# Kernel tuning notes

Hardware: AMD Instinct MI355X
Metric: run time of the kernel (lower is better)

Reference implementation:

```python
import jax, jax.numpy as jnp
import numpy as np

N_NODES = 500_000
N_EDGES = 8_000_000
N_GRAPHS = 512
N_FEATURES = 128
HIDDEN = 128
N_FILT = 8
OUT_DIM = 64
BN_EPS = 1e-5


def setup_inputs() -> dict:
    key = jax.random.key(0)
    ks = jax.random.split(key, 16)
    rn = lambda k, shape, s=0.05: jax.random.normal(k, shape, jnp.float32) * s
    return {
        "x": jax.random.normal(ks[0], (N_NODES, N_FEATURES), jnp.float32),
        "W1": rn(ks[1], (N_FEATURES, HIDDEN)),
        "b1": jnp.zeros((HIDDEN,), jnp.float32),
        "W2": rn(ks[2], (HIDDEN, N_FILT)),
        "b2": jnp.zeros((N_FILT,), jnp.float32),
        "W0": rn(ks[3], (2 * N_FILT, OUT_DIM)),
        "b0": jnp.zeros((OUT_DIM,), jnp.float32),
        "g1W": rn(ks[4], (OUT_DIM, OUT_DIM)),
        "g1b": jnp.zeros((OUT_DIM,), jnp.float32),
        "l1W": rn(ks[5], (OUT_DIM, OUT_DIM)),
        "g2W": rn(ks[6], (OUT_DIM, N_FEATURES)),
        "g2b": jnp.zeros((N_FEATURES,), jnp.float32),
        "l2W": rn(ks[7], (OUT_DIM, N_FEATURES)),
        "bn_gamma": jnp.ones((N_FEATURES,), jnp.float32),
        "bn_beta": jnp.zeros((N_FEATURES,), jnp.float32),
        "edge_index": jax.random.randint(ks[8], (2, N_EDGES), 0, N_NODES),
        "batch": jnp.sort(jax.random.randint(ks[9], (N_NODES,), 0, N_GRAPHS)),
        "death_edge_idx": jax.random.randint(ks[10], (N_NODES,), 0, N_EDGES),
    }


def _deepset(x, batch, GW, Gb, LW):
    # scatter-mean over graphs, Linear (no bias), gather-broadcast subtract
    sums = jax.ops.segment_sum(x, batch, num_segments=N_GRAPHS)  # [G, d]
    cnt = jax.ops.segment_sum(jnp.ones((x.shape[0], 1), x.dtype), batch,
                              num_segments=N_GRAPHS)             # [G, 1]
    xm = (sums / jnp.maximum(cnt, 1.0)) @ LW                      # Lambda
    return x @ GW + Gb - xm[batch]                                # Gamma - gather


def reference(x, W1, b1, W2, b2, W0, b0, g1W, g1b, l1W, g2W, g2b, l2W,
              bn_gamma, bn_beta, edge_index, batch, death_edge_idx):
    # filtrations MLP: [N, F] -> [N, n_filtrations]
    filtered_v = jax.nn.relu(x @ W1 + b1) @ W2 + b2
    # edge filtration = max of endpoint values (gather + max), [E, n_filtrations]
    filtered_e = jnp.maximum(filtered_v[edge_index[0]], filtered_v[edge_index[1]])
    # persistence pairs (lower-star 0-dim generators): birth = vertex value,
    # death = paired edge value; layout [N, n_filt, 2] -> [N, 2*n_filt]
    births = filtered_v
    deaths = filtered_e[death_edge_idx]
    x0 = jnp.stack([births, deaths], axis=-1).reshape(x.shape[0], 2 * N_FILT)
    # set_fn: Linear -> ReLU -> DeepSet -> ReLU -> DeepSet
    x0 = jax.nn.relu(x0 @ W0 + b0)
    x0 = jax.nn.relu(_deepset(x0, batch, g1W, g1b, l1W))
    x0 = _deepset(x0, batch, g2W, g2b, l2W)
    # residual: x + BatchNorm1d(relu(x0)) with batch statistics
    h = jax.nn.relu(x0)
    mu = h.mean(axis=0)
    var = h.var(axis=0)
    hn = (h - mu) * jax.lax.rsqrt(var + BN_EPS)
    return x + hn * bn_gamma + bn_beta
```

## Files before the change

kernel.cpp:

```cpp
#include <hip/hip_runtime.h>
#include <hip/hip_bf16.h>

#define NNODES 500000
#define NEDGES 8000000
#define NGRAPHS 512
#define NFEAT 128
#define NHID 128
#define NFILT 8
#define ODIM 64
#define BN_EPS 1e-5f
#define NBLK2 3907
#define NBLK3 7813

typedef __attribute__((ext_vector_type(8))) short bf16x8;
typedef __attribute__((ext_vector_type(4))) float f32x4;
#define MFMA16(a, b, c) __builtin_amdgcn_mfma_f32_16x16x32_bf16(a, b, c, 0, 0, 0)

__device__ inline ushort f2bs(float f) {
  union { __hip_bfloat16 h; ushort u; } cv;
  cv.h = __float2bfloat16(f);
  return cv.u;
}

__global__ void k_pack(const float* __restrict__ g1W, const float* __restrict__ g2W,
                       const float* __restrict__ W1,
                       ushort* __restrict__ pW1, ushort* __restrict__ pW2,
                       ushort* __restrict__ pW0) {
  int idx = blockIdx.x * 256 + threadIdx.x;
  if (idx < 4096) {
    int j = idx & 7, l = (idx >> 3) & 63, kb = (idx >> 9) & 1, ncb = idx >> 10;
    int k = kb * 32 + (l >> 4) * 8 + j, c = ncb * 16 + (l & 15);
    pW1[idx] = f2bs(g1W[k * 64 + c]);
  }
  if (idx < 8192) {
    int j = idx & 7, l = (idx >> 3) & 63, kb = (idx >> 9) & 1, ncb = idx >> 10;
    int k = kb * 32 + (l >> 4) * 8 + j, c = ncb * 16 + (l & 15);
    pW2[idx] = f2bs(g2W[k * 128 + c]);
  }
  if (idx < 16384) {
    int j = idx & 7, l = (idx >> 3) & 63, kb = (idx >> 9) & 3, ncb = idx >> 11;
    int k = kb * 32 + (l >> 4) * 8 + j, c = ncb * 16 + (l & 15);
    pW0[idx] = f2bs(W1[k * 128 + c]);
  }
}

__global__ __launch_bounds__(256) void k_filt(
    const float* __restrict__ x, const ushort* __restrict__ pW0,
    const float* __restrict__ b1, const float* __restrict__ W2,
    const float* __restrict__ b2, float* __restrict__ fv) {
  __shared__ float w2s[128 * 12];
  const int t = threadIdx.x;
  for (int i = t; i < 1024; i += 256) {
    int c = i >> 3, f = i & 7;
    w2s[c * 12 + f] = W2[i];
  }
  __syncthreads();
  const int wv = t >> 6, l = t & 63;
  const int lr = l & 15, lg = l >> 4;
  const int n0 = blockIdx.x * 128 + wv * 32;
  if (n0 >= NNODES) return;

  union { uint4 u; bf16x8 b; } bf[2][4];
#pragma unroll
  for (int mt = 0; mt < 2; ++mt)
#pragma unroll
    for (int kb = 0; kb < 4; ++kb) {
      const float* src = &x[(size_t)(n0 + mt * 16 + lr) * 128 + kb * 32 + lg * 8];
      float v[8];
      *(float4*)&v[0] = *(const float4*)src;
      *(float4*)&v[4] = *(const float4*)(src + 4);
      ushort s[8];
#pragma unroll
      for (int e = 0; e < 8; ++e) s[e] = f2bs(v[e]);
      bf[mt][kb].u = *(uint4*)s;
    }

  float pf0[8], pf1[8];
#pragma unroll
  for (int f = 0; f < 8; ++f) { pf0[f] = 0.f; pf1[f] = 0.f; }

#pragma unroll
  for (int ncb = 0; ncb < 8; ++ncb) {
    union { uint4 u; bf16x8 b; } af[4];
#pragma unroll
    for (int kb = 0; kb < 4; ++kb)
      af[kb].u = *(const uint4*)&pW0[((ncb * 4 + kb) * 64 + l) * 8];
    f32x4 a0 = (f32x4){0.f, 0.f, 0.f, 0.f};
    f32x4 a1 = (f32x4){0.f, 0.f, 0.f, 0.f};
#pragma unroll
    for (int kb = 0; kb < 4; ++kb) {
      a0 = MFMA16(af[kb].b, bf[0][kb].b, a0);
      a1 = MFMA16(af[kb].b, bf[1][kb].b, a1);
    }
    float bbv[4];
    *(float4*)bbv = *(const float4*)&b1[ncb * 16 + lg * 4];
#pragma unroll
    for (int r = 0; r < 4; ++r) {
      const int c = ncb * 16 + lg * 4 + r;
      float h0 = fmaxf(a0[r] + bbv[r], 0.f);
      float h1 = fmaxf(a1[r] + bbv[r], 0.f);
      float w20[4], w21[4];
      *(float4*)w20 = *(const float4*)&w2s[c * 12];
      *(float4*)w21 = *(const float4*)&w2s[c * 12 + 4];
#pragma unroll
      for (int f = 0; f < 4; ++f) {
        pf0[f]     = fmaf(h0, w20[f], pf0[f]);
        pf0[f + 4] = fmaf(h0, w21[f], pf0[f + 4]);
        pf1[f]     = fmaf(h1, w20[f], pf1[f]);
        pf1[f + 4] = fmaf(h1, w21[f], pf1[f + 4]);
      }
    }
  }
#pragma unroll
  for (int f = 0; f < 8; ++f) {
    pf0[f] += __shfl_xor(pf0[f], 16); pf0[f] += __shfl_xor(pf0[f], 32);
    pf1[f] += __shfl_xor(pf1[f], 16); pf1[f] += __shfl_xor(pf1[f], 32);
  }
  if (lg == 0) {
    float o0[8], o1[8];
#pragma unroll
    for (int f = 0; f < 8; ++f) {
      float bb = b2[f];
      o0[f] = pf0[f] + bb;
      o1[f] = pf1[f] + bb;
    }
    *(float4*)&fv[(size_t)(n0 + lr) * 8]          = *(float4*)&o0[0];
    *(float4*)&fv[(size_t)(n0 + lr) * 8 + 4]      = *(float4*)&o0[4];
    *(float4*)&fv[(size_t)(n0 + 16 + lr) * 8]     = *(float4*)&o1[0];
    *(float4*)&fv[(size_t)(n0 + 16 + lr) * 8 + 4] = *(float4*)&o1[4];
  }
}

__global__ void k_bounds(const int* __restrict__ batch, int* __restrict__ cnt) {
  int g = blockIdx.x * 64 + threadIdx.x;
  if (g >= NGRAPHS) return;
  int lo0 = 0, hi0 = NNODES;
  while (lo0 < hi0) { int mid = (lo0 + hi0) >> 1; if (batch[mid] < g) lo0 = mid + 1; else hi0 = mid; }
  int lo1 = lo0, hi1 = NNODES;
  while (lo1 < hi1) { int mid = (lo1 + hi1) >> 1; if (batch[mid] < g + 1) lo1 = mid + 1; else hi1 = mid; }
  cnt[g] = lo1 - lo0;
}

__global__ __launch_bounds__(256) void k_pairs(
    const float* __restrict__ fv, const int* __restrict__ edge_index,
    const int* __restrict__ didx, const int* __restrict__ batch,
    const float* __restrict__ W0, const float* __restrict__ b0,
    ushort* __restrict__ y, float* __restrict__ sums1) {
  __shared__ float w0s[16 * 64];
  __shared__ float b0s[64];
  __shared__ float ps[4][64];
  __shared__ int pg[4];
  const int t = threadIdx.x;
  for (int i = t; i < 1024; i += 256) w0s[i] = W0[i];
  if (t < 64) b0s[t] = b0[t];
  __syncthreads();

  const int wv = t >> 6, j = t & 63;
  const int n0 = blockIdx.x * 128 + wv * 32;

  int de = 0, gg = -1, uu = 0, vvx = 0;
  if (j < 32) {
    int nn = n0 + j;
    if (nn < NNODES) { de = didx[nn]; gg = batch[nn]; }
  }
  if (j < 32 && gg >= 0) { uu = edge_index[de]; vvx = edge_index[NEDGES + de]; }

  const float bb = b0s[j];
  float acc0 = 0.f, acc1 = 0.f;
  int g_first = -1, g_second = -1;

#pragma unroll 4
  for (int i = 0; i < 32; ++i) {
    int g = __shfl(gg, i);
    if (g >= 0) {
      int u = __shfl(uu, i);
      int v = __shfl(vvx, i);
      int n = n0 + i;
      float nb[8], ub[8], vb[8];
      *(float4*)&nb[0] = *(const float4*)&fv[(size_t)n * 8];
      *(float4*)&nb[4] = *(const float4*)&fv[(size_t)n * 8 + 4];
      *(float4*)&ub[0] = *(const float4*)&fv[(size_t)u * 8];
      *(float4*)&ub[4] = *(const float4*)&fv[(size_t)u * 8 + 4];
      *(float4*)&vb[0] = *(const float4*)&fv[(size_t)v * 8];
      *(float4*)&vb[4] = *(const float4*)&fv[(size_t)v * 8 + 4];
      float a = bb;
#pragma unroll
      for (int f = 0; f < 8; ++f) {
        a = fmaf(nb[f], w0s[(2 * f) * 64 + j], a);
        a = fmaf(fmaxf(ub[f], vb[f]), w0s[(2 * f + 1) * 64 + j], a);
      }
      a = fmaxf(a, 0.f);
      y[(size_t)n * 64 + j] = f2bs(a);
      if (g_first < 0) g_first = g;
      if (g == g_first) acc0 += a;
      else { g_second = g; acc1 += a; }
    }
  }
  if (g_second >= 0) atomicAdd(&sums1[g_second * 64 + j], acc1);
  ps[wv][j] = acc0;
  if (j == 0) pg[wv] = g_first;
  __syncthreads();

  if (t < 64) {
    const int bg = pg[0];
    float s = 0.f;
#pragma unroll
    for (int w = 0; w < 4; ++w) {
      const int gv = pg[w];
      if (gv < 0) continue;
      if (gv == bg) s += ps[w][t];
      else atomicAdd(&sums1[gv * 64 + t], ps[w][t]);
    }
    if (bg >= 0) atomicAdd(&sums1[bg * 64 + t], s);
  }
}

template <int D>
__global__ void k_meanlin(const float* __restrict__ sums,
                          const int* __restrict__ cnt,
                          const float* __restrict__ LW,
                          float* __restrict__ xm) {
  __shared__ float m[64];
  const int g = blockIdx.x, t = threadIdx.x;
  const float c = fmaxf((float)cnt[g], 1.f);
  if (t < 64) m[t] = sums[g * 64 + t] / c;
  __syncthreads();
  float a = 0.f;
#pragma unroll
  for (int k = 0; k < 64; ++k) a = fmaf(m[k], LW[k * D + t], a);
  xm[g * D + t] = a;
}

__global__ __launch_bounds__(256) void k_ds1(
    const ushort* __restrict__ ybf, const int* __restrict__ batch,
    const ushort* __restrict__ pW1, const float* __restrict__ g1b,
    const float* __restrict__ xm1, ushort* __restrict__ y2,
    float* __restrict__ sums2) {
  __shared__ ushort ys[128 * 132];
  __shared__ float ps[4][64];
  __shared__ int pg[4];
  const int t = threadIdx.x, wv = t >> 6, l = t & 63;
  const int lr = l & 15, lg = l >> 4, c0 = lg * 4;
  const int nblk = blockIdx.x * 128;
  const int rmax = min(128, NNODES - nblk);

  const uint4* srcp = (const uint4*)(ybf + (size_t)nblk * 64);
  for (int i = t; i < rmax * 8; i += 256) {
    int row = i >> 3, c8 = i & 7;
    *(uint4*)&ys[row * 132 + c8 * 8] = srcp[i];
  }
  __syncthreads();

  const int n0 = nblk + wv * 32;
  if (n0 < NNODES) {
    union { uint4 u; bf16x8 b; } bf[2][2];
#pragma unroll
    for (int mt = 0; mt < 2; ++mt)
#pragma unroll
      for (int kb = 0; kb < 2; ++kb)
        bf[mt][kb].u = *(const uint4*)&ys[(wv * 32 + mt * 16 + lr) * 132 + kb * 32 + lg * 8];

    union { uint4 u; bf16x8 b; } af[4][2];
#pragma unroll
    for (int ncb = 0; ncb < 4; ++ncb)
#pragma unroll
      for (int kb = 0; kb < 2; ++kb)
        af[ncb][kb].u = *(const uint4*)&pW1[((ncb * 2 + kb) * 64 + l) * 8];

    f32x4 acc[2][4];
#pragma unroll
    for (int mt = 0; mt < 2; ++mt)
#pragma unroll
      for (int ncb = 0; ncb < 4; ++ncb) {
        acc[mt][ncb] = (f32x4){0.f, 0.f, 0.f, 0.f};
        acc[mt][ncb] = MFMA16(af[ncb][0].b, bf[mt][0].b, acc[mt][ncb]);
        acc[mt][ncb] = MFMA16(af[ncb][1].b, bf[mt][1].b, acc[mt][ncb]);
      }

    const int g0 = batch[n0 + lr], g1 = batch[n0 + 16 + lr];
    const int g_first = __shfl(g0, 0);

    float wsum[4][4];
#pragma unroll
    for (int ncb = 0; ncb < 4; ++ncb)
#pragma unroll
      for (int r = 0; r < 4; ++r) wsum[ncb][r] = 0.f;

#pragma unroll
    for (int mt = 0; mt < 2; ++mt) {
      const int g = mt ? g1 : g0;
      const int row = wv * 32 + mt * 16 + lr;
      const bool prim = (g == g_first);
#pragma unroll
      for (int ncb = 0; ncb < 4; ++ncb) {
        const int c = ncb * 16 + c0;
        float xmv[4], bbv[4];
        *(float4*)xmv = *(const float4*)&xm1[g * 64 + c];
        *(float4*)bbv = *(const float4*)&g1b[c];
        ushort st[4];
#pragma unroll
        for (int r = 0; r < 4; ++r) {
          float v = fmaxf(acc[mt][ncb][r] + bbv[r] - xmv[r], 0.f);
          st[r] = f2bs(v);
          if (prim) wsum[ncb][r] += v;
          else atomicAdd(&sums2[g * 64 + c + r], v);
        }
        *(ushort4*)&ys[row * 132 + c] = *(ushort4*)st;
      }
    }
#pragma unroll
    for (int ncb = 0; ncb < 4; ++ncb)
#pragma unroll
      for (int r = 0; r < 4; ++r) {
        float w = wsum[ncb][r];
        w += __shfl_xor(w, 1); w += __shfl_xor(w, 2);
        w += __shfl_xor(w, 4); w += __shfl_xor(w, 8);
        if (lr == 0) ps[wv][ncb * 16 + c0 + r] = w;
      }
    if (l == 0) pg[wv] = g_first;
  } else {
    ps[wv][l] = 0.f;
    if (l == 0) pg[wv] = -1;
  }
  __syncthreads();

  if (t < 64) {
    const int bg = pg[0];
    float s = 0.f;
#pragma unroll
    for (int w = 0; w < 4; ++w) {
      const int gv = pg[w];
      if (gv < 0) continue;
      if (gv == bg) s += ps[w][t];
      else atomicAdd(&sums2[gv * 64 + t], ps[w][t]);
    }
    if (bg >= 0) atomicAdd(&sums2[bg * 64 + t], s);
  }

  uint4* dstp = (uint4*)(y2 + (size_t)nblk * 64);
  for (int i = t; i < rmax * 8; i += 256) {
    int row = i >> 3, c8 = i & 7;
    dstp[i] = *(const uint4*)&ys[row * 132 + c8 * 8];
  }
}

__global__ __launch_bounds__(256) void k_ds2a(
    const ushort* __restrict__ y2, const int* __restrict__ batch,
    const ushort* __restrict__ pW2, const float* __restrict__ g2b,
    const float* __restrict__ xm2,
    float* __restrict__ pmu, float* __restrict__ psq) {
  __shared__ ushort ys[128 * 132];
  __shared__ float ps[4][128], pq[4][128];
  const int t = threadIdx.x, wv = t >> 6, l = t & 63;
  const int lr = l & 15, lg = l >> 4, c0 = lg * 4;
  const int nblk = blockIdx.x * 128;
  const int rmax = min(128, NNODES - nblk);

  const uint4* srcp = (const uint4*)(y2 + (size_t)nblk * 64);
  for (int i = t; i < rmax * 8; i += 256) {
    int row = i >> 3, c8 = i & 7;
    *(uint4*)&ys[row * 132 + c8 * 8] = srcp[i];
  }
  __syncthreads();

  const int n0r = nblk + wv * 32;
  const bool act = n0r < NNODES;
  const int n0 = act ? n0r : 0;
  const int rbase = act ? wv * 32 : 0;

  union { uint4 u; bf16x8 b; } bf[2][2];
#pragma unroll
  for (int mt = 0; mt < 2; ++mt)
#pragma unroll
    for (int kb = 0; kb < 2; ++kb)
      bf[mt][kb].u = *(const uint4*)&ys[(rbase + mt * 16 + lr) * 132 + kb * 32 + lg * 8];

  const int g0 = batch[n0 + lr], g1 = batch[n0 + 16 + lr];

#pragma unroll
  for (int ncb = 0; ncb < 8; ++ncb) {
    union { uint4 u; bf16x8 b; } af0, af1;
    af0.u = *(const uint4*)&pW2[((ncb * 2 + 0) * 64 + l) * 8];
    af1.u = *(const uint4*)&pW2[((ncb * 2 + 1) * 64 + l) * 8];
    f32x4 a0 = (f32x4){0.f, 0.f, 0.f, 0.f}, a1 = (f32x4){0.f, 0.f, 0.f, 0.f};
    a0 = MFMA16(af0.b, bf[0][0].b, a0); a0 = MFMA16(af1.b, bf[0][1].b, a0);
    a1 = MFMA16(af0.b, bf[1][0].b, a1); a1 = MFMA16(af1.b, bf[1][1].b, a1);

    const int c = ncb * 16 + c0;
    float xm0[4], xm1v[4], bbv[4];
    *(float4*)xm0 = *(const float4*)&xm2[g0 * 128 + c];
    *(float4*)xm1v = *(const float4*)&xm2[g1 * 128 + c];
    *(float4*)bbv = *(const float4*)&g2b[c];
    float w[4], q[4];
#pragma unroll
    for (int r = 0; r < 4; ++r) {
      float v0 = fmaxf(a0[r] + bbv[r] - xm0[r], 0.f);
      float v1 = fmaxf(a1[r] + bbv[r] - xm1v[r], 0.f);
      if (!act) { v0 = 0.f; v1 = 0.f; }
      w[r] = v0 + v1;
      q[r] = fmaf(v0, v0, v1 * v1);
    }
#pragma unroll
    for (int r = 0; r < 4; ++r) {
      float wr = w[r], qr = q[r];
      wr += __shfl_xor(wr, 1); wr += __shfl_xor(wr, 2);
      wr += __shfl_xor(wr, 4); wr += __shfl_xor(wr, 8);
      qr += __shfl_xor(qr, 1); qr += __shfl_xor(qr, 2);
      qr += __shfl_xor(qr, 4); qr += __shfl_xor(qr, 8);
      if (lr == 0) { ps[wv][c + r] = wr; pq[wv][c + r] = qr; }
    }
  }
  __syncthreads();
  if (t < 128) {
    pmu[(size_t)blockIdx.x * 128 + t] = ps[0][t] + ps[1][t] + ps[2][t] + ps[3][t];
    psq[(size_t)blockIdx.x * 128 + t] = pq[0][t] + pq[1][t] + pq[2][t] + pq[3][t];
  }
}

__global__ void k_red(const float* __restrict__ pmu, const float* __restrict__ psq,
                      float* __restrict__ musum, float* __restrict__ sqsum) {
  const int f = threadIdx.x & 127;
  const bool mu = threadIdx.x < 128;
  const float* src = mu ? pmu : psq;
  float s = 0.f;
  for (int b = blockIdx.x; b < NBLK2; b += 32) s += src[(size_t)b * 128 + f];
  atomicAdd(mu ? &musum[f] : &sqsum[f], s);
}

__global__ __launch_bounds__(256) void k_bn(
    const ushort* __restrict__ y2, const int* __restrict__ batch,
    const ushort* __restrict__ pW2, const float* __restrict__ g2b,
    const float* __restrict__ xm2, const float* __restrict__ x,
    const float* __restrict__ musum, const float* __restrict__ sqsum,
    const float* __restrict__ gamma, const float* __restrict__ beta,
    float* __restrict__ out) {
  __shared__ float vs[64 * 132];
  __shared__ float smu[128], ssc[128], sbe[128];
  const int t = threadIdx.x, wv = t >> 6, l = t & 63;
  const int lr = l & 15, lg = l >> 4, c0 = lg * 4;
  if (t < 128) {
    const float invN = 1.f / (float)NNODES;
    float m = musum[t] * invN;
    float v = sqsum[t] * invN - m * m;
    smu[t] = m;
    ssc[t] = rsqrtf(v + BN_EPS) * gamma[t];
    sbe[t] = beta[t];
  }
  const int nblk = blockIdx.x * 64;
  const int n0 = nblk + wv * 16;

  if (n0 < NNODES) {
    union { uint4 u; bf16x8 b; } bf[2];
#pragma unroll
    for (int kb = 0; kb < 2; ++kb)
      bf[kb].u = *(const uint4*)&y2[(size_t)(n0 + lr) * 64 + kb * 32 + lg * 8];

    const int g0 = batch[n0 + lr];
    const int row0 = wv * 16 + lr;

#pragma unroll
    for (int ncb = 0; ncb < 8; ++ncb) {
      union { uint4 u; bf16x8 b; } af0, af1;
      af0.u = *(const uint4*)&pW2[((ncb * 2 + 0) * 64 + l) * 8];
      af1.u = *(const uint4*)&pW2[((ncb * 2 + 1) * 64 + l) * 8];
      f32x4 a0 = (f32x4){0.f, 0.f, 0.f, 0.f};
      a0 = MFMA16(af0.b, bf[0].b, a0);
      a0 = MFMA16(af1.b, bf[1].b, a0);

      const int c = ncb * 16 + c0;
      float bbv[4], xm0[4], hvv[4];
      *(float4*)bbv = *(const float4*)&g2b[c];
      *(float4*)xm0 = *(const float4*)&xm2[g0 * 128 + c];
#pragma unroll
      for (int r = 0; r < 4; ++r)
        hvv[r] = fmaxf(a0[r] + bbv[r] - xm0[r], 0.f);
      *(float4*)&vs[row0 * 132 + c] = *(float4*)hvv;
    }
  }
  __syncthreads();

  const int rmax = NNODES - nblk;
  for (int i = t; i < 2048; i += 256) {
    const int row = i >> 5, c4 = (i & 31) * 4;
    if (row >= rmax) break;
    const int n = nblk + row;
    float hv[4], muv[4], scv[4], bev[4], xv[4], o[4];
    *(float4*)hv = *(const float4*)&vs[row * 132 + c4];
    *(float4*)muv = *(const float4*)&smu[c4];
    *(float4*)scv = *(const float4*)&ssc[c4];
    *(float4*)bev = *(const float4*)&sbe[c4];
    *(float4*)xv = *(const float4*)&x[(size_t)n * 128 + c4];
#pragma unroll
    for (int r = 0; r < 4; ++r)
      o[r] = xv[r] + (hv[r] - muv[r]) * scv[r] + bev[r];
    *(float4*)&out[(size_t)n * 128 + c4] = *(float4*)o;
  }
}

extern "C" void kernel_launch(void* const* d_in, const int* in_sizes, int n_in,
                              void* d_out, int out_size, void* d_ws,
                              size_t ws_size, hipStream_t stream) {
  const float* x     = (const float*)d_in[0];
  const float* W1    = (const float*)d_in[1];
  const float* b1    = (const float*)d_in[2];
  const float* W2    = (const float*)d_in[3];
  const float* b2    = (const float*)d_in[4];
  const float* W0    = (const float*)d_in[5];
  const float* b0    = (const float*)d_in[6];
  const float* g1W   = (const float*)d_in[7];
  const float* g1b   = (const float*)d_in[8];
  const float* l1W   = (const float*)d_in[9];
  const float* g2W   = (const float*)d_in[10];
  const float* g2b   = (const float*)d_in[11];
  const float* l2W   = (const float*)d_in[12];
  const float* gamma = (const float*)d_in[13];
  const float* beta  = (const float*)d_in[14];
  const int* edge_index = (const int*)d_in[15];
  const int* batch      = (const int*)d_in[16];
  const int* didx       = (const int*)d_in[17];
  float* out = (float*)d_out;

  char* ws = (char*)d_ws;
  float*  fv    = (float*) (ws + 0);
  float*  pmu   = (float*) (ws + 0);
  float*  psq   = (float*) (ws + 2000384);
  ushort* ybf   = (ushort*)(ws + 16000000);
  ushort* y2    = (ushort*)(ws + 80000000);
  float*  sums1 = (float*) (ws + 144000000);
  float*  sums2 = (float*) (ws + 144131072);
  float*  musum = (float*) (ws + 144262144);
  float*  sqsum = (float*) (ws + 144262656);
  int*    cnt   = (int*)   (ws + 144263168);
  float*  xm1   = (float*) (ws + 144265216);
  float*  xm2   = (float*) (ws + 144396288);
  ushort* pW1   = (ushort*)(ws + 144658432);
  ushort* pW2   = (ushort*)(ws + 144666624);
  ushort* pW0   = (ushort*)(ws + 144683008);

  hipMemsetAsync(ws + 144000000, 0, 263168, stream);

  k_pack<<<64, 256, 0, stream>>>(g1W, g2W, W1, pW1, pW2, pW0);
  k_bounds<<<8, 64, 0, stream>>>(batch, cnt);
  k_filt<<<NBLK2, 256, 0, stream>>>(x, pW0, b1, W2, b2, fv);
  k_pairs<<<NBLK2, 256, 0, stream>>>(fv, edge_index, didx, batch, W0, b0, ybf, sums1);
  k_meanlin<64><<<NGRAPHS, 64, 0, stream>>>(sums1, cnt, l1W, xm1);
  k_ds1<<<NBLK2, 256, 0, stream>>>(ybf, batch, pW1, g1b, xm1, y2, sums2);
  k_meanlin<128><<<NGRAPHS, 128, 0, stream>>>(sums2, cnt, l2W, xm2);
  k_ds2a<<<NBLK2, 256, 0, stream>>>(y2, batch, pW2, g2b, xm2, pmu, psq);
  k_red<<<32, 256, 0, stream>>>(pmu, psq, musum, sqsum);
  k_bn<<<NBLK3, 256, 0, stream>>>(y2, batch, pW2, g2b, xm2, x, musum, sqsum,
                                  gamma, beta, out);
}
```

Measured before the change: 551.2 us.

## Process four node tiles per block in deepset kernels and fold bounds into pack

k_ds1 and k_ds2a now each cover 512 nodes per block (977 blocks) instead of 128. They loop over four tiles, load the weight fragments once and read activations straight from global memory rather than staging them through LDS. k_ds2a keeps its per-thread BN partial sums in registers across tiles, which shrinks the partial arrays k_red has to reduce. The graph-bounds binary search moves into k_pack, removing one launch. The costs are fewer blocks to spread across the GPU, a register-heavier ds2a, and unstaged global loads and stores of 8-byte pieces per lane in ds1.

New measurement: 541.3 us. About the same (-1.8%).

```diff
diff --git a/kernel.cpp b/kernel.cpp
--- a/kernel.cpp
+++ b/kernel.cpp
@@ -11,6 +11,7 @@
 #define BN_EPS 1e-5f
 #define NBLK2 3907
 #define NBLK3 7813
+#define NBLK4 977
 
 typedef __attribute__((ext_vector_type(8))) short bf16x8;
 typedef __attribute__((ext_vector_type(4))) float f32x4;
@@ -23,9 +24,9 @@
 }
 
 __global__ void k_pack(const float* __restrict__ g1W, const float* __restrict__ g2W,
-                       const float* __restrict__ W1,
+                       const float* __restrict__ W1, const int* __restrict__ batch,
                        ushort* __restrict__ pW1, ushort* __restrict__ pW2,
-                       ushort* __restrict__ pW0) {
+                       ushort* __restrict__ pW0, int* __restrict__ cnt) {
   int idx = blockIdx.x * 256 + threadIdx.x;
   if (idx < 4096) {
     int j = idx & 7, l = (idx >> 3) & 63, kb = (idx >> 9) & 1, ncb = idx >> 10;
@@ -41,6 +42,14 @@
     int j = idx & 7, l = (idx >> 3) & 63, kb = (idx >> 9) & 3, ncb = idx >> 11;
     int k = kb * 32 + (l >> 4) * 8 + j, c = ncb * 16 + (l & 15);
     pW0[idx] = f2bs(W1[k * 128 + c]);
+  }
+  if (idx < NGRAPHS) {
+    int g = idx;
+    int lo0 = 0, hi0 = NNODES;
+    while (lo0 < hi0) { int mid = (lo0 + hi0) >> 1; if (batch[mid] < g) lo0 = mid + 1; else hi0 = mid; }
+    int lo1 = lo0, hi1 = NNODES;
+    while (lo1 < hi1) { int mid = (lo1 + hi1) >> 1; if (batch[mid] < g + 1) lo1 = mid + 1; else hi1 = mid; }
+    cnt[g] = lo1 - lo0;
   }
 }
 
@@ -129,16 +138,6 @@
     *(float4*)&fv[(size_t)(n0 + 16 + lr) * 8]     = *(float4*)&o1[0];
     *(float4*)&fv[(size_t)(n0 + 16 + lr) * 8 + 4] = *(float4*)&o1[4];
   }
-}
-
-__global__ void k_bounds(const int* __restrict__ batch, int* __restrict__ cnt) {
-  int g = blockIdx.x * 64 + threadIdx.x;
-  if (g >= NGRAPHS) return;
-  int lo0 = 0, hi0 = NNODES;
-  while (lo0 < hi0) { int mid = (lo0 + hi0) >> 1; if (batch[mid] < g) lo0 = mid + 1; else hi0 = mid; }
-  int lo1 = lo0, hi1 = NNODES;
-  while (lo1 < hi1) { int mid = (lo1 + hi1) >> 1; if (batch[mid] < g + 1) lo1 = mid + 1; else hi1 = mid; }
-  cnt[g] = lo1 - lo0;
 }
 
 __global__ __launch_bounds__(256) void k_pairs(
@@ -236,111 +235,99 @@
     const ushort* __restrict__ pW1, const float* __restrict__ g1b,
     const float* __restrict__ xm1, ushort* __restrict__ y2,
     float* __restrict__ sums2) {
-  __shared__ ushort ys[128 * 132];
   __shared__ float ps[4][64];
   __shared__ int pg[4];
   const int t = threadIdx.x, wv = t >> 6, l = t & 63;
   const int lr = l & 15, lg = l >> 4, c0 = lg * 4;
-  const int nblk = blockIdx.x * 128;
-  const int rmax = min(128, NNODES - nblk);
-
-  const uint4* srcp = (const uint4*)(ybf + (size_t)nblk * 64);
-  for (int i = t; i < rmax * 8; i += 256) {
-    int row = i >> 3, c8 = i & 7;
-    *(uint4*)&ys[row * 132 + c8 * 8] = srcp[i];
-  }
-  __syncthreads();
-
-  const int n0 = nblk + wv * 32;
-  if (n0 < NNODES) {
-    union { uint4 u; bf16x8 b; } bf[2][2];
-#pragma unroll
-    for (int mt = 0; mt < 2; ++mt)
-#pragma unroll
-      for (int kb = 0; kb < 2; ++kb)
-        bf[mt][kb].u = *(const uint4*)&ys[(wv * 32 + mt * 16 + lr) * 132 + kb * 32 + lg * 8];
-
-    union { uint4 u; bf16x8 b; } af[4][2];
-#pragma unroll
-    for (int ncb = 0; ncb < 4; ++ncb)
-#pragma unroll
-      for (int kb = 0; kb < 2; ++kb)
-        af[ncb][kb].u = *(const uint4*)&pW1[((ncb * 2 + kb) * 64 + l) * 8];
-
-    f32x4 acc[2][4];
-#pragma unroll
-    for (int mt = 0; mt < 2; ++mt)
-#pragma unroll
-      for (int ncb = 0; ncb < 4; ++ncb) {
-        acc[mt][ncb] = (f32x4){0.f, 0.f, 0.f, 0.f};
-        acc[mt][ncb] = MFMA16(af[ncb][0].b, bf[mt][0].b, acc[mt][ncb]);
-        acc[mt][ncb] = MFMA16(af[ncb][1].b, bf[mt][1].b, acc[mt][ncb]);
+  const int nbase = blockIdx.x * 512;
+
+  union { uint4 u; bf16x8 b; } af[4][2];
+#pragma unroll
+  for (int ncb = 0; ncb < 4; ++ncb)
+#pragma unroll
+    for (int kb = 0; kb < 2; ++kb)
+      af[ncb][kb].u = *(const uint4*)&pW1[((ncb * 2 + kb) * 64 + l) * 8];
+
+  for (int tile = 0; tile < 4; ++tile) {
+    const int n0 = nbase + tile * 128 + wv * 32;
+    if (n0 < NNODES) {
+      union { uint4 u; bf16x8 b; } bf[2][2];
+#pragma unroll
+      for (int mt = 0; mt < 2; ++mt)
+#pragma unroll
+        for (int kb = 0; kb < 2; ++kb)
+          bf[mt][kb].u = *(const uint4*)&ybf[(size_t)(n0 + mt * 16 + lr) * 64 + kb * 32 + lg * 8];
+
+      f32x4 acc[2][4];
+#pragma unroll
+      for (int mt = 0; mt < 2; ++mt)
+#pragma unroll
+        for (int ncb = 0; ncb < 4; ++ncb) {
+          acc[mt][ncb] = (f32x4){0.f, 0.f, 0.f, 0.f};
+          acc[mt][ncb] = MFMA16(af[ncb][0].b, bf[mt][0].b, acc[mt][ncb]);
+          acc[mt][ncb] = MFMA16(af[ncb][1].b, bf[mt][1].b, acc[mt][ncb]);
+        }
+
+      const int g0 = batch[n0 + lr], g1 = batch[n0 + 16 + lr];
+      const int g_first = __shfl(g0, 0);
+
+      float wsum[4][4];
+#pragma unroll
+      for (int ncb = 0; ncb < 4; ++ncb)
+#pragma unroll
+        for (int r = 0; r < 4; ++r) wsum[ncb][r] = 0.f;
+
+#pragma unroll
+      for (int mt = 0; mt < 2; ++mt) {
+        const int n = n0 + mt * 16 + lr;
+        const int g = mt ? g1 : g0;
+        const bool prim = (g == g_first);
+#pragma unroll
+        for (int ncb = 0; ncb < 4; ++ncb) {
+          const int c = ncb * 16 + c0;
+          float xmv[4], bbv[4];
+          *(float4*)xmv = *(const float4*)&xm1[g * 64 + c];
+          *(float4*)bbv = *(const float4*)&g1b[c];
+          ushort st[4];
+#pragma unroll
+          for (int r = 0; r < 4; ++r) {
+            float v = fmaxf(acc[mt][ncb][r] + bbv[r] - xmv[r], 0.f);
+            st[r] = f2bs(v);
+            if (prim) wsum[ncb][r] += v;
+            else atomicAdd(&sums2[g * 64 + c + r], v);
+          }
+          *(ushort4*)&y2[(size_t)n * 64 + c] = *(ushort4*)st;
+        }
       }
-
-    const int g0 = batch[n0 + lr], g1 = batch[n0 + 16 + lr];
-    const int g_first = __shfl(g0, 0);
-
-    float wsum[4][4];
-#pragma unroll
-    for (int ncb = 0; ncb < 4; ++ncb)
-#pragma unroll
-      for (int r = 0; r < 4; ++r) wsum[ncb][r] = 0.f;
-
-#pragma unroll
-    for (int mt = 0; mt < 2; ++mt) {
-      const int g = mt ? g1 : g0;
-      const int row = wv * 32 + mt * 16 + lr;
-      const bool prim = (g == g_first);
-#pragma unroll
-      for (int ncb = 0; ncb < 4; ++ncb) {
-        const int c = ncb * 16 + c0;
-        float xmv[4], bbv[4];
-        *(float4*)xmv = *(const float4*)&xm1[g * 64 + c];
-        *(float4*)bbv = *(const float4*)&g1b[c];
-        ushort st[4];
+#pragma unroll
+      for (int ncb = 0; ncb < 4; ++ncb)
 #pragma unroll
         for (int r = 0; r < 4; ++r) {
-          float v = fmaxf(acc[mt][ncb][r] + bbv[r] - xmv[r], 0.f);
-          st[r] = f2bs(v);
-          if (prim) wsum[ncb][r] += v;
-          else atomicAdd(&sums2[g * 64 + c + r], v);
+          float w = wsum[ncb][r];
+          w += __shfl_xor(w, 1); w += __shfl_xor(w, 2);
+          w += __shfl_xor(w, 4); w += __shfl_xor(w, 8);
+          if (lr == 0) ps[wv][ncb * 16 + c0 + r] = w;
         }
-        *(ushort4*)&ys[row * 132 + c] = *(ushort4*)st;
+      if (l == 0) pg[wv] = g_first;
+    } else {
+      ps[wv][l] = 0.f;
+      if (l == 0) pg[wv] = -1;
+    }
+    __syncthreads();
+
+    if (t < 64) {
+      const int bg = pg[0];
+      float s = 0.f;
+#pragma unroll
+      for (int w = 0; w < 4; ++w) {
+        const int gv = pg[w];
+        if (gv < 0) continue;
+        if (gv == bg) s += ps[w][t];
+        else atomicAdd(&sums2[gv * 64 + t], ps[w][t]);
       }
-    }
-#pragma unroll
-    for (int ncb = 0; ncb < 4; ++ncb)
-#pragma unroll
-      for (int r = 0; r < 4; ++r) {
-        float w = wsum[ncb][r];
-        w += __shfl_xor(w, 1); w += __shfl_xor(w, 2);
-        w += __shfl_xor(w, 4); w += __shfl_xor(w, 8);
-        if (lr == 0) ps[wv][ncb * 16 + c0 + r] = w;
-      }
-    if (l == 0) pg[wv] = g_first;
-  } else {
-    ps[wv][l] = 0.f;
-    if (l == 0) pg[wv] = -1;
-  }
-  __syncthreads();
-
-  if (t < 64) {
-    const int bg = pg[0];
-    float s = 0.f;
-#pragma unroll
-    for (int w = 0; w < 4; ++w) {
-      const int gv = pg[w];
-      if (gv < 0) continue;
-      if (gv == bg) s += ps[w][t];
-      else atomicAdd(&sums2[gv * 64 + t], ps[w][t]);
-    }
-    if (bg >= 0) atomicAdd(&sums2[bg * 64 + t], s);
-  }
-
-  uint4* dstp = (uint4*)(y2 + (size_t)nblk * 64);
-  for (int i = t; i < rmax * 8; i += 256) {
-    int row = i >> 3, c8 = i & 7;
-    dstp[i] = *(const uint4*)&ys[row * 132 + c8 * 8];
+      if (bg >= 0) atomicAdd(&sums2[bg * 64 + t], s);
+    }
+    __syncthreads();
   }
 }
 
@@ -349,67 +336,65 @@
     const ushort* __restrict__ pW2, const float* __restrict__ g2b,
     const float* __restrict__ xm2,
     float* __restrict__ pmu, float* __restrict__ psq) {
-  __shared__ ushort ys[128 * 132];
   __shared__ float ps[4][128], pq[4][128];
   const int t = threadIdx.x, wv = t >> 6, l = t & 63;
   const int lr = l & 15, lg = l >> 4, c0 = lg * 4;
-  const int nblk = blockIdx.x * 128;
-  const int rmax = min(128, NNODES - nblk);
-
-  const uint4* srcp = (const uint4*)(y2 + (size_t)nblk * 64);
-  for (int i = t; i < rmax * 8; i += 256) {
-    int row = i >> 3, c8 = i & 7;
-    *(uint4*)&ys[row * 132 + c8 * 8] = srcp[i];
-  }
-  __syncthreads();
-
-  const int n0r = nblk + wv * 32;
-  const bool act = n0r < NNODES;
-  const int n0 = act ? n0r : 0;
-  const int rbase = act ? wv * 32 : 0;
-
-  union { uint4 u; bf16x8 b; } bf[2][2];
-#pragma unroll
-  for (int mt = 0; mt < 2; ++mt)
-#pragma unroll
-    for (int kb = 0; kb < 2; ++kb)
-      bf[mt][kb].u = *(const uint4*)&ys[(rbase + mt * 16 + lr) * 132 + kb * 32 + lg * 8];
-
-  const int g0 = batch[n0 + lr], g1 = batch[n0 + 16 + lr];
-
-#pragma unroll
-  for (int ncb = 0; ncb < 8; ++ncb) {
-    union { uint4 u; bf16x8 b; } af0, af1;
-    af0.u = *(const uint4*)&pW2[((ncb * 2 + 0) * 64 + l) * 8];
-    af1.u = *(const uint4*)&pW2[((ncb * 2 + 1) * 64 + l) * 8];
-    f32x4 a0 = (f32x4){0.f, 0.f, 0.f, 0.f}, a1 = (f32x4){0.f, 0.f, 0.f, 0.f};
-    a0 = MFMA16(af0.b, bf[0][0].b, a0); a0 = MFMA16(af1.b, bf[0][1].b, a0);
-    a1 = MFMA16(af0.b, bf[1][0].b, a1); a1 = MFMA16(af1.b, bf[1][1].b, a1);
-
-    const int c = ncb * 16 + c0;
-    float xm0[4], xm1v[4], bbv[4];
-    *(float4*)xm0 = *(const float4*)&xm2[g0 * 128 + c];
-    *(float4*)xm1v = *(const float4*)&xm2[g1 * 128 + c];
-    *(float4*)bbv = *(const float4*)&g2b[c];
-    float w[4], q[4];
+  const int nbase = blockIdx.x * 512;
+
+  float sw[8][4], sq[8][4];
+#pragma unroll
+  for (int ncb = 0; ncb < 8; ++ncb)
+#pragma unroll
+    for (int r = 0; r < 4; ++r) { sw[ncb][r] = 0.f; sq[ncb][r] = 0.f; }
+
+  for (int tile = 0; tile < 4; ++tile) {
+    const int n0 = nbase + tile * 128 + wv * 32;
+    if (n0 >= NNODES) continue;
+
+    union { uint4 u; bf16x8 b; } bf[2][2];
+#pragma unroll
+    for (int mt = 0; mt < 2; ++mt)
+#pragma unroll
+      for (int kb = 0; kb < 2; ++kb)
+        bf[mt][kb].u = *(const uint4*)&y2[(size_t)(n0 + mt * 16 + lr) * 64 + kb * 32 + lg * 8];
+
+    const int g0 = batch[n0 + lr], g1 = batch[n0 + 16 + lr];
+
+#pragma unroll
+    for (int ncb = 0; ncb < 8; ++ncb) {
+      union { uint4 u; bf16x8 b; } af0, af1;
+      af0.u = *(const uint4*)&pW2[((ncb * 2 + 0) * 64 + l) * 8];
+      af1.u = *(const uint4*)&pW2[((ncb * 2 + 1) * 64 + l) * 8];
+      f32x4 a0 = (f32x4){0.f, 0.f, 0.f, 0.f}, a1 = (f32x4){0.f, 0.f, 0.f, 0.f};
+      a0 = MFMA16(af0.b, bf[0][0].b, a0); a0 = MFMA16(af1.b, bf[0][1].b, a0);
+      a1 = MFMA16(af0.b, bf[1][0].b, a1); a1 = MFMA16(af1.b, bf[1][1].b, a1);
+
+      const int c = ncb * 16 + c0;
+      float xm0[4], xm1v[4], bbv[4];
+      *(float4*)xm0 = *(const float4*)&xm2[g0 * 128 + c];
+      *(float4*)xm1v = *(const float4*)&xm2[g1 * 128 + c];
+      *(float4*)bbv = *(const float4*)&g2b[c];
+#pragma unroll
+      for (int r = 0; r < 4; ++r) {
+        float v0 = fmaxf(a0[r] + bbv[r] - xm0[r], 0.f);
+        float v1 = fmaxf(a1[r] + bbv[r] - xm1v[r], 0.f);
+        sw[ncb][r] += v0 + v1;
+        sq[ncb][r] = fmaf(v0, v0, fmaf(v1, v1, sq[ncb][r]));
+      }
+    }
+  }
+
+#pragma unroll
+  for (int ncb = 0; ncb < 8; ++ncb)
 #pragma unroll
     for (int r = 0; r < 4; ++r) {
-      float v0 = fmaxf(a0[r] + bbv[r] - xm0[r], 0.f);
-      float v1 = fmaxf(a1[r] + bbv[r] - xm1v[r], 0.f);
-      if (!act) { v0 = 0.f; v1 = 0.f; }
-      w[r] = v0 + v1;
-      q[r] = fmaf(v0, v0, v1 * v1);
-    }
-#pragma unroll
-    for (int r = 0; r < 4; ++r) {
-      float wr = w[r], qr = q[r];
+      float wr = sw[ncb][r], qr = sq[ncb][r];
       wr += __shfl_xor(wr, 1); wr += __shfl_xor(wr, 2);
       wr += __shfl_xor(wr, 4); wr += __shfl_xor(wr, 8);
       qr += __shfl_xor(qr, 1); qr += __shfl_xor(qr, 2);
       qr += __shfl_xor(qr, 4); qr += __shfl_xor(qr, 8);
-      if (lr == 0) { ps[wv][c + r] = wr; pq[wv][c + r] = qr; }
-    }
-  }
+      if (lr == 0) { ps[wv][ncb * 16 + c0 + r] = wr; pq[wv][ncb * 16 + c0 + r] = qr; }
+    }
   __syncthreads();
   if (t < 128) {
     pmu[(size_t)blockIdx.x * 128 + t] = ps[0][t] + ps[1][t] + ps[2][t] + ps[3][t];
@@ -423,7 +408,7 @@
   const bool mu = threadIdx.x < 128;
   const float* src = mu ? pmu : psq;
   float s = 0.f;
-  for (int b = blockIdx.x; b < NBLK2; b += 32) s += src[(size_t)b * 128 + f];
+  for (int b = blockIdx.x; b < NBLK4; b += 32) s += src[(size_t)b * 128 + f];
   atomicAdd(mu ? &musum[f] : &sqsum[f], s);
 }
 
@@ -539,14 +524,13 @@
 
   hipMemsetAsync(ws + 144000000, 0, 263168, stream);
 
-  k_pack<<<64, 256, 0, stream>>>(g1W, g2W, W1, pW1, pW2, pW0);
-  k_bounds<<<8, 64, 0, stream>>>(batch, cnt);
+  k_pack<<<64, 256, 0, stream>>>(g1W, g2W, W1, batch, pW1, pW2, pW0, cnt);
   k_filt<<<NBLK2, 256, 0, stream>>>(x, pW0, b1, W2, b2, fv);
   k_pairs<<<NBLK2, 256, 0, stream>>>(fv, edge_index, didx, batch, W0, b0, ybf, sums1);
   k_meanlin<64><<<NGRAPHS, 64, 0, stream>>>(sums1, cnt, l1W, xm1);
-  k_ds1<<<NBLK2, 256, 0, stream>>>(ybf, batch, pW1, g1b, xm1, y2, sums2);
+  k_ds1<<<NBLK4, 256, 0, stream>>>(ybf, batch, pW1, g1b, xm1, y2, sums2);
   k_meanlin<128><<<NGRAPHS, 128, 0, stream>>>(sums2, cnt, l2W, xm2);
-  k_ds2a<<<NBLK2, 256, 0, stream>>>(y2, batch, pW2, g2b, xm2, pmu, psq);
+  k_ds2a<<<NBLK4, 256, 0, stream>>>(y2, batch, pW2, g2b, xm2, pmu, psq);
   k_red<<<32, 256, 0, stream>>>(pmu, psq, musum, sqsum);
   k_bn<<<NBLK3, 256, 0, stream>>>(y2, batch, pW2, g2b, xm2, x, musum, sqsum,
                                   gamma, beta, out);
```
